# Performance work log

Measured on AMD Instinct MI355X. Metric: run time of the kernel, lower is better.

Reference implementation:

```python
import jax, jax.numpy as jnp
import numpy as np

N_NODES = 100_000
N_EDGES = 1_600_000
HIDDEN = 32


def setup_inputs() -> dict:
    key = jax.random.key(0)
    ks = jax.random.split(key, 8)
    pos = jax.random.normal(ks[0], (N_NODES, 3), dtype=jnp.float32)
    edge_index = jax.random.randint(ks[1], (2, N_EDGES), 0, N_NODES, dtype=jnp.int64)
    batch = jnp.zeros((N_NODES,), dtype=jnp.int64)
    # layer 1 MLP: Linear(3+3 -> 32) -> ReLU -> Linear(32 -> 32)
    W1 = jax.random.normal(ks[2], (6, HIDDEN), dtype=jnp.float32) * (1.0 / np.sqrt(6))
    b1 = jnp.zeros((HIDDEN,), dtype=jnp.float32)
    W2 = jax.random.normal(ks[3], (HIDDEN, HIDDEN), dtype=jnp.float32) * (1.0 / np.sqrt(HIDDEN))
    b2 = jnp.zeros((HIDDEN,), dtype=jnp.float32)
    # layer 2 MLP: Linear(32+3 -> 32) -> ReLU -> Linear(32 -> 32)
    W3 = jax.random.normal(ks[4], (HIDDEN + 3, HIDDEN), dtype=jnp.float32) * (1.0 / np.sqrt(HIDDEN + 3))
    b3 = jnp.zeros((HIDDEN,), dtype=jnp.float32)
    W4 = jax.random.normal(ks[5], (HIDDEN, HIDDEN), dtype=jnp.float32) * (1.0 / np.sqrt(HIDDEN))
    b4 = jnp.zeros((HIDDEN,), dtype=jnp.float32)
    return {"pos": pos, "edge_index": edge_index, "batch": batch,
            "W1": W1, "b1": b1, "W2": W2, "b2": b2,
            "W3": W3, "b3": b3, "W4": W4, "b4": b4}


def _pointnet_layer(h, rel, src, dst, n_nodes, Wa, ba, Wb, bb):
    # per-edge: concat(h_j, pos_j - pos_i) -> Linear -> ReLU -> Linear, then max-scatter into i
    e = jnp.concatenate([h[src], rel], axis=-1)             # [E, in+3]
    m = jax.nn.relu(e @ Wa + ba) @ Wb + bb                  # [E, out]
    agg = jax.ops.segment_max(m, dst, num_segments=n_nodes)  # [N, out], -inf for isolated nodes
    return jnp.where(jnp.isfinite(agg), agg, 0.0)


def reference(pos, edge_index, batch, W1, b1, W2, b2, W3, b3, W4, b4):
    src = edge_index[0]  # j (source)
    dst = edge_index[1]  # i (target, aggregation index)
    n_nodes = pos.shape[0]
    rel = pos[src] - pos[dst]  # [E, 3]
    h = jax.nn.relu(_pointnet_layer(pos, rel, src, dst, n_nodes, W1, b1, W2, b2))
    h = jax.nn.relu(_pointnet_layer(h, rel, src, dst, n_nodes, W3, b3, W4, b4))
    return h
```

## Files before the change

kernel.cpp:

```cpp
#include <hip/hip_runtime.h>
#include <hip/hip_bf16.h>
#include <stdint.h>


#define BS 256
#define EBS 512
#define K1_EDGES 4096
#define RB 64
#define RCAP 2048

typedef float v2f __attribute__((ext_vector_type(2)));
typedef __attribute__((ext_vector_type(8))) short bf16x8;
typedef __attribute__((ext_vector_type(16))) float f32x16;
typedef __bf16 bf16v2 __attribute__((ext_vector_type(2)));

#define SRC_MASK 0xFFFFFu

__device__ __forceinline__ unsigned cvt2(float x, float y) {
    v2f v = {x, y};
    bf16v2 b = __builtin_convertvector(v, bf16v2);
    return __builtin_bit_cast(unsigned, b);
}
__device__ __forceinline__ float bflo(unsigned u) { return __uint_as_float(u << 16); }
__device__ __forceinline__ float bfhi(unsigned u) { return __uint_as_float(u & 0xFFFF0000u); }

__device__ __forceinline__ uint4 mk_frag(uint4 ua, float4 v0, float4 v1) {
    const v2f z = {0.0f, 0.0f};
    uint4 o;
    v2f a;
    a = (v2f){bflo(ua.x), bfhi(ua.x)} - (v2f){v0.x, v0.y};
    a = __builtin_elementwise_max(a, z);
    o.x = cvt2(a.x, a.y);
    a = (v2f){bflo(ua.y), bfhi(ua.y)} - (v2f){v0.z, v0.w};
    a = __builtin_elementwise_max(a, z);
    o.y = cvt2(a.x, a.y);
    a = (v2f){bflo(ua.z), bfhi(ua.z)} - (v2f){v1.x, v1.y};
    a = __builtin_elementwise_max(a, z);
    o.z = cvt2(a.x, a.y);
    a = (v2f){bflo(ua.w), bfhi(ua.w)} - (v2f){v1.z, v1.w};
    a = __builtin_elementwise_max(a, z);
    o.w = cvt2(a.x, a.y);
    return o;
}

__global__ __launch_bounds__(BS) void setup_kernel(
    const float* __restrict__ pos, const float* __restrict__ Wa, const float* __restrict__ ba,
    unsigned* __restrict__ Ubf, float* __restrict__ V, int N, int NBn, int NRP,
    const float* __restrict__ Wb2, const float* __restrict__ Wb4,
    unsigned* __restrict__ WbtG, int* __restrict__ cnt) {
    const int tid = threadIdx.x;
    const int b = blockIdx.x;
    if (b < NBn) {
        const int n = b * BS + tid;
        if (n >= N) return;
        const float p[3] = {pos[3 * n], pos[3 * n + 1], pos[3 * n + 2]};
        v2f u[16], v[16];
#pragma unroll
        for (int g = 0; g < 16; ++g) {
            u[g] = *reinterpret_cast<const v2f*>(&ba[g * 2]);
            v2f z = {0.0f, 0.0f};
            v[g] = z;
        }
#pragma unroll
        for (int i = 0; i < 3; ++i) {
            const v2f f = {p[i], p[i]};
#pragma unroll
            for (int g = 0; g < 16; ++g) {
                const v2f wA = *reinterpret_cast<const v2f*>(&Wa[i * 32 + g * 2]);
                const v2f wB = *reinterpret_cast<const v2f*>(&Wa[(i + 3) * 32 + g * 2]);
                u[g] = __builtin_elementwise_fma(f, wA + wB, u[g]);
                v[g] = __builtin_elementwise_fma(f, wB, v[g]);
            }
        }
        uint4* Up = reinterpret_cast<uint4*>(Ubf + (size_t)n * 16);
        float4* Vp = reinterpret_cast<float4*>(V + (size_t)n * 32);
#pragma unroll
        for (int q = 0; q < 4; ++q) {
            uint4 o;
            o.x = cvt2(u[4 * q + 0].x, u[4 * q + 0].y);
            o.y = cvt2(u[4 * q + 1].x, u[4 * q + 1].y);
            o.z = cvt2(u[4 * q + 2].x, u[4 * q + 2].y);
            o.w = cvt2(u[4 * q + 3].x, u[4 * q + 3].y);
            Up[q] = o;
        }
#pragma unroll
        for (int q = 0; q < 8; ++q)
            Vp[q] = make_float4(v[2 * q].x, v[2 * q].y, v[2 * q + 1].x, v[2 * q + 1].y);
    } else {
        if (tid < 128) {
            const int layer = tid >> 6;
            const int t = tid & 63;
            const int lnp = t & 31;
            const int hp = t >> 5;
            const float* Wb = layer ? Wb4 : Wb2;
            unsigned* dst = WbtG + layer * 512 + t * 8;
#pragma unroll
            for (int q = 0; q < 4; ++q) {
                const int p = 4 * hp + q;
                dst[q] = cvt2(Wb[(2 * p) * 32 + lnp], Wb[(2 * p + 1) * 32 + lnp]);
                dst[4 + q] = cvt2(Wb[(2 * p + 16) * 32 + lnp], Wb[(2 * p + 17) * 32 + lnp]);
            }
        }
        for (int r = tid; r < NRP; r += BS) cnt[r] = 0;
    }
}

__global__ __launch_bounds__(BS) void bucket_scatter_kernel(
    const int* __restrict__ ei, int E, int NRP, int* __restrict__ cnt,
    unsigned* __restrict__ sedgeB) {
    __shared__ unsigned stage[K1_EDGES];
    __shared__ unsigned short rng[K1_EDGES];
    __shared__ unsigned short inv[K1_EDGES];
    __shared__ int hist[2048], startL[2048], cursor[2048];
    __shared__ int ts[BS];
    const int tid = threadIdx.x;
    for (int r = tid; r < 2048; r += BS) hist[r] = 0;
    __syncthreads();
    const int base = blockIdx.x * K1_EDGES;
    const int M = min(K1_EDGES, E - base);
    for (int i = tid; i < M; i += BS) {
        const int src = ei[base + i];
        const int dst = ei[E + base + i];
        const int r = dst >> 6;
        stage[i] = (unsigned)src | ((unsigned)(dst & 63) << 20);
        rng[i] = (unsigned short)r;
        atomicAdd(&hist[r], 1);
    }
    __syncthreads();
    {
        const int i0 = tid * 8;
        int lv[8];
        int tsum = 0;
#pragma unroll
        for (int k = 0; k < 8; ++k) {
            lv[k] = hist[i0 + k];
            tsum += lv[k];
        }
        ts[tid] = tsum;
        __syncthreads();
        for (int off2 = 1; off2 < BS; off2 <<= 1) {
            int add = (tid >= off2) ? ts[tid - off2] : 0;
            __syncthreads();
            ts[tid] += add;
            __syncthreads();
        }
        int run = ts[tid] - tsum;
#pragma unroll
        for (int k = 0; k < 8; ++k) {
            startL[i0 + k] = run;
            cursor[i0 + k] = run;
            run += lv[k];
        }
    }
    __syncthreads();
    for (int i = tid; i < M; i += BS) {
        const int pos = atomicAdd(&cursor[rng[i]], 1);
        inv[pos] = (unsigned short)i;
    }
    __syncthreads();
    for (int r = tid; r < 2048; r += BS) {
        const int h = hist[r];
        if (h > 0) cursor[r] = atomicAdd(&cnt[r], h);
    }
    __syncthreads();
    for (int j = tid; j < M; j += BS) {
        const int i = inv[j];
        const int r = rng[i];
        sedgeB[((size_t)r << 11) + cursor[r] + (j - startL[r])] = stage[i];
    }
}

template <int MODE>
__global__ __launch_bounds__(EBS, 6) void edge_range_kernel(
    const unsigned* __restrict__ Ubf, const float4* __restrict__ V,
    const unsigned* __restrict__ sedgeB, const int* __restrict__ cnt,
    const unsigned* __restrict__ WbtG,
    const float* __restrict__ bb, const float* __restrict__ pos,
    const float* __restrict__ Wa2, const float* __restrict__ ba2,
    unsigned* __restrict__ Ubf2, float* __restrict__ Vbuf2,
    float* __restrict__ out, int N) {
    __shared__ unsigned aggL[2048];
    __shared__ __align__(16) float4 vlds[576];
    __shared__ unsigned dstw[8][16];

    const int tid = threadIdx.x;
    const int r = blockIdx.x;
    const size_t base = (size_t)r << 11;
    const int M = min(cnt[r], RCAP);
    const int last = M - 1;

    const int l = tid & 63;
    const int w = tid >> 6;
    const int half = l >> 5;
    const int ln = l & 31;

#pragma unroll
    for (int i = 0; i < 4; ++i) aggL[tid + i * EBS] = 0u;

    {
        const float4* Vg = V + ((size_t)r << 9);
        const int vmax = min(512, (N - (r << 6)) * 8);
        if (tid < vmax) vlds[(tid >> 3) * 9 + (tid & 7)] = Vg[tid];
    }

    const uint4 bu0 = *reinterpret_cast<const uint4*>(WbtG + l * 8);
    const uint4 bu1 = *reinterpret_cast<const uint4*>(WbtG + l * 8 + 4);
    const float bbn = bb[ln];
    __syncthreads();

    const int nch = (M + EBS - 1) >> 9;
    unsigned pk = 0;
    if (64 * w < M) pk = sedgeB[base + min(64 * w + l, last)];
    for (int c = 0; c < nch; ++c) {
        unsigned npk = 0;
        const int ncb = (c + 1) << 9;
        const bool nextAct = (c + 1 < nch) && (ncb + 64 * w < M);
        if (nextAct) npk = sedgeB[base + min(ncb + 64 * w + l, last)];
        if ((c << 9) + 64 * w < M) {
            reinterpret_cast<unsigned char*>(dstw[w])[l] = (unsigned char)(pk >> 20);

            const unsigned pkA = __shfl(pk, ln, 64);
            const unsigned pkB = __shfl(pk, 32 + ln, 64);
            uint4 au00, au01, au10, au11;
            {
                const uint4* Up = reinterpret_cast<const uint4*>(Ubf + (size_t)(pkA & SRC_MASK) * 16);
                const float4* Vr = &vlds[(pkA >> 20) * 9];
                au00 = mk_frag(Up[half], Vr[2 * half], Vr[2 * half + 1]);
                au01 = mk_frag(Up[2 + half], Vr[4 + 2 * half], Vr[5 + 2 * half]);
            }
            {
                const uint4* Up = reinterpret_cast<const uint4*>(Ubf + (size_t)(pkB & SRC_MASK) * 16);
                const float4* Vr = &vlds[(pkB >> 20) * 9];
                au10 = mk_frag(Up[half], Vr[2 * half], Vr[2 * half + 1]);
                au11 = mk_frag(Up[2 + half], Vr[4 + 2 * half], Vr[5 + 2 * half]);
            }

            f32x16 c0, c1;
#pragma unroll
            for (int i = 0; i < 16; ++i) {
                c0[i] = bbn;
                c1[i] = bbn;
            }
            c0 = __builtin_amdgcn_mfma_f32_32x32x16_bf16(
                __builtin_bit_cast(bf16x8, au00), __builtin_bit_cast(bf16x8, bu0), c0, 0, 0, 0);
            c0 = __builtin_amdgcn_mfma_f32_32x32x16_bf16(
                __builtin_bit_cast(bf16x8, au01), __builtin_bit_cast(bf16x8, bu1), c0, 0, 0, 0);
            c1 = __builtin_amdgcn_mfma_f32_32x32x16_bf16(
                __builtin_bit_cast(bf16x8, au10), __builtin_bit_cast(bf16x8, bu0), c1, 0, 0, 0);
            c1 = __builtin_amdgcn_mfma_f32_32x32x16_bf16(
                __builtin_bit_cast(bf16x8, au11), __builtin_bit_cast(bf16x8, bu1), c1, 0, 0, 0);

            const unsigned* dw = dstw[w];
#pragma unroll
            for (int g = 0; g < 4; ++g) {
                const unsigned p0 = dw[2 * g + half];
                const unsigned p1 = dw[8 + 2 * g + half];
                {
                    const float v0 = c0[4 * g + 0], v1 = c0[4 * g + 1];
                    const float v2 = c0[4 * g + 2], v3 = c0[4 * g + 3];
                    if (p0 == (p0 & 0xFFu) * 0x01010101u) {
                        const float m = fmaxf(fmaxf(v0, v1), fmaxf(v2, v3));
                        atomicMax(&aggL[((p0 & 0x3Fu) << 5) | ln],
                                  __float_as_uint(fmaxf(m, 0.0f)));
                    } else {
                        atomicMax(&aggL[(((p0 >> 0) & 0x3Fu) << 5) | ln],
                                  __float_as_uint(fmaxf(v0, 0.0f)));
                        atomicMax(&aggL[(((p0 >> 8) & 0x3Fu) << 5) | ln],
                                  __float_as_uint(fmaxf(v1, 0.0f)));
                        atomicMax(&aggL[(((p0 >> 16) & 0x3Fu) << 5) | ln],
                                  __float_as_uint(fmaxf(v2, 0.0f)));
                        atomicMax(&aggL[(((p0 >> 24) & 0x3Fu) << 5) | ln],
                                  __float_as_uint(fmaxf(v3, 0.0f)));
                    }
                }
                {
                    const float v0 = c1[4 * g + 0], v1 = c1[4 * g + 1];
                    const float v2 = c1[4 * g + 2], v3 = c1[4 * g + 3];
                    if (p1 == (p1 & 0xFFu) * 0x01010101u) {
                        const float m = fmaxf(fmaxf(v0, v1), fmaxf(v2, v3));
                        atomicMax(&aggL[((p1 & 0x3Fu) << 5) | ln],
                                  __float_as_uint(fmaxf(m, 0.0f)));
                    } else {
                        atomicMax(&aggL[(((p1 >> 0) & 0x3Fu) << 5) | ln],
                                  __float_as_uint(fmaxf(v0, 0.0f)));
                        atomicMax(&aggL[(((p1 >> 8) & 0x3Fu) << 5) | ln],
                                  __float_as_uint(fmaxf(v1, 0.0f)));
                        atomicMax(&aggL[(((p1 >> 16) & 0x3Fu) << 5) | ln],
                                  __float_as_uint(fmaxf(v2, 0.0f)));
                        atomicMax(&aggL[(((p1 >> 24) & 0x3Fu) << 5) | ln],
                                  __float_as_uint(fmaxf(v3, 0.0f)));
                    }
                }
            }
        }
        pk = npk;
    }
    __syncthreads();

    if (MODE == 0) {
        const int idx = tid * 4;
        const int node = (r << 6) + (idx >> 5);
        if (node < N) {
            float4 o;
            o.x = __uint_as_float(aggL[idx + 0]);
            o.y = __uint_as_float(aggL[idx + 1]);
            o.z = __uint_as_float(aggL[idx + 2]);
            o.w = __uint_as_float(aggL[idx + 3]);
            *reinterpret_cast<float4*>(out + (size_t)node * 32 + (idx & 31)) = o;
        }
    } else {
        const int node_l = tid >> 3;
        const int qq = tid & 7;
        const int node = (r << 6) + node_l;
        if (node < N) {
            const unsigned* row = &aggL[node_l << 5];
            float h[32];
#pragma unroll
            for (int i = 0; i < 32; ++i) h[i] = __uint_as_float(row[i]);
            const float pp[3] = {pos[3 * node], pos[3 * node + 1], pos[3 * node + 2]};
            v2f u[2], v[2];
#pragma unroll
            for (int g = 0; g < 2; ++g) {
                u[g] = *reinterpret_cast<const v2f*>(&ba2[4 * qq + 2 * g]);
                v2f z = {0.0f, 0.0f};
                v[g] = z;
            }
#pragma unroll
            for (int i = 0; i < 32; ++i) {
                const v2f f = {h[i], h[i]};
#pragma unroll
                for (int g = 0; g < 2; ++g) {
                    const v2f wv =
                        *reinterpret_cast<const v2f*>(&Wa2[i * 32 + 4 * qq + 2 * g]);
                    u[g] = __builtin_elementwise_fma(f, wv, u[g]);
                }
            }
#pragma unroll
            for (int i = 0; i < 3; ++i) {
                const v2f f = {pp[i], pp[i]};
#pragma unroll
                for (int g = 0; g < 2; ++g) {
                    const v2f wv =
                        *reinterpret_cast<const v2f*>(&Wa2[(32 + i) * 32 + 4 * qq + 2 * g]);
                    u[g] = __builtin_elementwise_fma(f, wv, u[g]);
                    v[g] = __builtin_elementwise_fma(f, wv, v[g]);
                }
            }
            uint2 o;
            o.x = cvt2(u[0].x, u[0].y);
            o.y = cvt2(u[1].x, u[1].y);
            *reinterpret_cast<uint2*>(Ubf2 + (size_t)node * 16 + 2 * qq) = o;
            *reinterpret_cast<float4*>(Vbuf2 + (size_t)node * 32 + 4 * qq) =
                make_float4(v[0].x, v[0].y, v[1].x, v[1].y);
        }
    }
}

extern "C" void kernel_launch(void* const* d_in, const int* in_sizes, int n_in,
                              void* d_out, int out_size, void* d_ws, size_t ws_size,
                              hipStream_t stream) {
    const float* pos = (const float*)d_in[0];
    const int* ei = (const int*)d_in[1];
    const float* W1 = (const float*)d_in[3];
    const float* b1 = (const float*)d_in[4];
    const float* W2 = (const float*)d_in[5];
    const float* b2 = (const float*)d_in[6];
    const float* W3 = (const float*)d_in[7];
    const float* b3 = (const float*)d_in[8];
    const float* W4 = (const float*)d_in[9];
    const float* b4 = (const float*)d_in[10];

    const int E = in_sizes[1] / 2;
    const int N = in_sizes[0] / 3;
    const int n32 = N * 32;
    const int NPAD = ((N + BS - 1) / BS) * BS;
    const int NR = (N + RB - 1) / RB;
    const int NRP = ((NR + 15) / 16) * 16;
    const int NB1 = (E + K1_EDGES - 1) / K1_EDGES;

    int* cnt = (int*)d_ws;
    unsigned* sedgeB = (unsigned*)(cnt + NRP);
    unsigned* Ubf = sedgeB + ((size_t)NR << 11);
    float* Vbuf = (float*)(Ubf + (size_t)NPAD * 16);
    unsigned* Ubf2 = (unsigned*)(Vbuf + n32);
    float* Vbuf2 = (float*)(Ubf2 + (size_t)NPAD * 16);
    unsigned* WbtG = (unsigned*)(Vbuf2 + n32);

    const int NBn = (N + BS - 1) / BS;

    setup_kernel<<<NBn + 1, BS, 0, stream>>>(pos, W1, b1, Ubf, Vbuf, N, NBn, NRP, W2, W4,
                                             WbtG, cnt);
    bucket_scatter_kernel<<<NB1, BS, 0, stream>>>(ei, E, NRP, cnt, sedgeB);

    edge_range_kernel<1><<<NR, EBS, 0, stream>>>(Ubf, (const float4*)Vbuf, sedgeB, cnt, WbtG,
                                                 b2, pos, W3, b3, Ubf2, Vbuf2, nullptr, N);
    edge_range_kernel<0><<<NR, EBS, 0, stream>>>(Ubf2, (const float4*)Vbuf2, sedgeB, cnt,
                                                 WbtG + 512, b4, nullptr, nullptr, nullptr,
                                                 nullptr, nullptr, (float*)d_out, N);
}
```

Baseline: 194.0 us.

## Merge bucket scatter into setup kernel and drop local prefix-sum sort

Fuses the edge bucket-scatter work and the per-node setup work into one frontend kernel launch, with the counter zeroing moved to a hipMemsetAsync beforehand. The bucket scatter drops its block-local prefix scan and inverse permutation and instead claims slots directly with shared-memory atomics on the cursor. This removes one kernel launch, several barriers and the scan. In exchange, writes within a bucket are no longer contiguous or ordered, and a capacity guard (RCAP) now silently drops edges that overflow a bucket.

```diff
diff --git a/kernel.cpp b/kernel.cpp
--- a/kernel.cpp
+++ b/kernel.cpp
@@ -43,15 +43,44 @@
     return o;
 }
 
-__global__ __launch_bounds__(BS) void setup_kernel(
+__global__ __launch_bounds__(BS) void frontend_kernel(
+    const int* __restrict__ ei, int E, int* __restrict__ cnt,
+    unsigned* __restrict__ sedgeB,
     const float* __restrict__ pos, const float* __restrict__ Wa, const float* __restrict__ ba,
-    unsigned* __restrict__ Ubf, float* __restrict__ V, int N, int NBn, int NRP,
+    unsigned* __restrict__ Ubf, float* __restrict__ V, int N, int NB1, int NBn,
     const float* __restrict__ Wb2, const float* __restrict__ Wb4,
-    unsigned* __restrict__ WbtG, int* __restrict__ cnt) {
+    unsigned* __restrict__ WbtG) {
+    __shared__ unsigned stage[K1_EDGES];
+    __shared__ unsigned short rng[K1_EDGES];
+    __shared__ int hist[2048], cursor[2048];
     const int tid = threadIdx.x;
     const int b = blockIdx.x;
-    if (b < NBn) {
-        const int n = b * BS + tid;
+    if (b < NB1) {
+        for (int r = tid; r < 2048; r += BS) hist[r] = 0;
+        __syncthreads();
+        const int base = b * K1_EDGES;
+        const int M = min(K1_EDGES, E - base);
+        for (int i = tid; i < M; i += BS) {
+            const int src = ei[base + i];
+            const int dst = ei[E + base + i];
+            const int r = dst >> 6;
+            stage[i] = (unsigned)src | ((unsigned)(dst & 63) << 20);
+            rng[i] = (unsigned short)r;
+            atomicAdd(&hist[r], 1);
+        }
+        __syncthreads();
+        for (int r = tid; r < 2048; r += BS) {
+            const int h = hist[r];
+            if (h > 0) cursor[r] = atomicAdd(&cnt[r], h);
+        }
+        __syncthreads();
+        for (int i = tid; i < M; i += BS) {
+            const int r = rng[i];
+            const int slot = atomicAdd(&cursor[r], 1);
+            if (slot < RCAP) sedgeB[((size_t)r << 11) + slot] = stage[i];
+        }
+    } else if (b < NB1 + NBn) {
+        const int n = (b - NB1) * BS + tid;
         if (n >= N) return;
         const float p[3] = {pos[3 * n], pos[3 * n + 1], pos[3 * n + 2]};
         v2f u[16], v[16];
@@ -101,72 +130,6 @@
                 dst[4 + q] = cvt2(Wb[(2 * p + 16) * 32 + lnp], Wb[(2 * p + 17) * 32 + lnp]);
             }
         }
-        for (int r = tid; r < NRP; r += BS) cnt[r] = 0;
-    }
-}
-
-__global__ __launch_bounds__(BS) void bucket_scatter_kernel(
-    const int* __restrict__ ei, int E, int NRP, int* __restrict__ cnt,
-    unsigned* __restrict__ sedgeB) {
-    __shared__ unsigned stage[K1_EDGES];
-    __shared__ unsigned short rng[K1_EDGES];
-    __shared__ unsigned short inv[K1_EDGES];
-    __shared__ int hist[2048], startL[2048], cursor[2048];
-    __shared__ int ts[BS];
-    const int tid = threadIdx.x;
-    for (int r = tid; r < 2048; r += BS) hist[r] = 0;
-    __syncthreads();
-    const int base = blockIdx.x * K1_EDGES;
-    const int M = min(K1_EDGES, E - base);
-    for (int i = tid; i < M; i += BS) {
-        const int src = ei[base + i];
-        const int dst = ei[E + base + i];
-        const int r = dst >> 6;
-        stage[i] = (unsigned)src | ((unsigned)(dst & 63) << 20);
-        rng[i] = (unsigned short)r;
-        atomicAdd(&hist[r], 1);
-    }
-    __syncthreads();
-    {
-        const int i0 = tid * 8;
-        int lv[8];
-        int tsum = 0;
-#pragma unroll
-        for (int k = 0; k < 8; ++k) {
-            lv[k] = hist[i0 + k];
-            tsum += lv[k];
-        }
-        ts[tid] = tsum;
-        __syncthreads();
-        for (int off2 = 1; off2 < BS; off2 <<= 1) {
-            int add = (tid >= off2) ? ts[tid - off2] : 0;
-            __syncthreads();
-            ts[tid] += add;
-            __syncthreads();
-        }
-        int run = ts[tid] - tsum;
-#pragma unroll
-        for (int k = 0; k < 8; ++k) {
-            startL[i0 + k] = run;
-            cursor[i0 + k] = run;
-            run += lv[k];
-        }
-    }
-    __syncthreads();
-    for (int i = tid; i < M; i += BS) {
-        const int pos = atomicAdd(&cursor[rng[i]], 1);
-        inv[pos] = (unsigned short)i;
-    }
-    __syncthreads();
-    for (int r = tid; r < 2048; r += BS) {
-        const int h = hist[r];
-        if (h > 0) cursor[r] = atomicAdd(&cnt[r], h);
-    }
-    __syncthreads();
-    for (int j = tid; j < M; j += BS) {
-        const int i = inv[j];
-        const int r = rng[i];
-        sedgeB[((size_t)r << 11) + cursor[r] + (j - startL[r])] = stage[i];
     }
 }
 
@@ -388,9 +351,9 @@
 
     const int NBn = (N + BS - 1) / BS;
 
-    setup_kernel<<<NBn + 1, BS, 0, stream>>>(pos, W1, b1, Ubf, Vbuf, N, NBn, NRP, W2, W4,
-                                             WbtG, cnt);
-    bucket_scatter_kernel<<<NB1, BS, 0, stream>>>(ei, E, NRP, cnt, sedgeB);
+    hipMemsetAsync(cnt, 0, (size_t)NRP * sizeof(int), stream);
+    frontend_kernel<<<NB1 + NBn + 1, BS, 0, stream>>>(ei, E, cnt, sedgeB, pos, W1, b1, Ubf,
+                                                      Vbuf, N, NB1, NBn, W2, W4, WbtG);
 
     edge_range_kernel<1><<<NR, EBS, 0, stream>>>(Ubf, (const float4*)Vbuf, sedgeB, cnt, WbtG,
                                                  b2, pos, W3, b3, Ubf2, Vbuf2, nullptr, N);
```

Measured after the change: 188.8 us, median of 2. 2.7% less time.
